# Performance work log

Hardware: AMD Instinct MI355X
Metric: run time of the kernel (lower is better)

## Reference

```python
import jax, jax.numpy as jnp
import numpy as np
import math

B, S, DM, H, N_HASHES, BUCKET = 1, 1024, 512, 8, 8, 64
HD = DM // H
N_BUCKETS = max(2, 2 * (S // (2 * BUCKET)))   # 16
ROT = max(1, N_BUCKETS // 2)                  # 8


def setup_inputs() -> dict:
    key = jax.random.key(0)
    ks = jax.random.split(key, 6)
    sc = 1.0 / math.sqrt(DM)
    return {
        "x": jax.random.normal(ks[0], (B, S, DM), dtype=jnp.float32),
        "w_qk": (jax.random.normal(ks[1], (DM, DM), dtype=jnp.float32) * sc),
        "b_qk": jnp.zeros((DM,), dtype=jnp.float32),
        "w_v": (jax.random.normal(ks[2], (DM, DM), dtype=jnp.float32) * sc),
        "b_v": jnp.zeros((DM,), dtype=jnp.float32),
        "w_o": (jax.random.normal(ks[3], (DM, DM), dtype=jnp.float32) * sc),
        "b_o": jnp.zeros((DM,), dtype=jnp.float32),
        # random rotations used for LSH hashing (torch.randn in hash_vectors)
        "rotations": jax.random.normal(ks[4], (N_HASHES, H, HD, ROT), dtype=jnp.float32),
    }


def reference(x, w_qk, b_qk, w_v, b_v, w_o, b_o, rotations):
    # projections, split heads: (B, H, S, HD)
    qk = (x @ w_qk + b_qk).reshape(B, S, H, HD).transpose(0, 2, 1, 3)
    v = (x @ w_v + b_v).reshape(B, S, H, HD).transpose(0, 2, 1, 3)

    # LSH bucket assignment: (B, H, S, n_hashes)
    rot = jnp.einsum('bhnd,rhdc->bhnrc', qk, rotations)
    rot = jnp.concatenate([rot, -rot], axis=-1)
    buckets = jnp.argmax(rot, axis=-1)

    # The original gathers (batch, head, pos) jointly per bucket, so attention
    # mixes across batch and head; flatten exactly the same way.
    N = B * H * S
    qkf = qk.reshape(N, HD)
    vf = v.reshape(N, HD)
    bkf = buckets.reshape(N, N_HASHES).T  # (n_hashes, N)

    # dots are shared across hash rounds; only the bucket mask changes
    dots = (qkf @ qkf.T) / math.sqrt(HD)  # (N, N)

    def body(acc, bk):
        same = bk[:, None] == bk[None, :]  # bucket-equality mask
        w = jax.nn.softmax(jnp.where(same, dots, -jnp.inf), axis=-1)
        return acc + w @ vf, None

    out, _ = jax.lax.scan(body, jnp.zeros_like(vf), bkf)
    out = out / N_HASHES

    out = out.reshape(B, H, S, HD).transpose(0, 2, 1, 3).reshape(B, S, DM)
    return out @ w_o + b_o
```

## Files before the change

kernel.cpp:

```cpp
#include <hip/hip_runtime.h>
#include <math.h>

#define S 1024
#define DM 512
#define H 8
#define HD 64
#define NH 8
#define NB 16
#define N 8192
#define SCALE 0.125f
#define EXP2C 0.18033688f

typedef __attribute__((ext_vector_type(4))) float f32x4;
typedef __attribute__((ext_vector_type(8))) short s16x8;
typedef __attribute__((ext_vector_type(4))) short s16x4;

__device__ __forceinline__ short f2bf(float f) {
  union { float f; unsigned u; } a; a.f = f;
  unsigned r = a.u + 0x7fffu + ((a.u >> 16) & 1u);
  return (short)(r >> 16);
}
__device__ __forceinline__ float bf2f(short h) {
  union { unsigned u; float f; } a; a.u = ((unsigned)(unsigned short)h) << 16;
  return a.f;
}
__device__ __forceinline__ int f2bf2(float lo, float hi) {
  return (int)(unsigned short)f2bf(lo) | (((int)f2bf(hi)) << 16);
}

#if __has_builtin(__builtin_amdgcn_mfma_f32_16x16x16_bf16)
#define MFMA_PV(a, b, c) __builtin_amdgcn_mfma_f32_16x16x16_bf16(a, b, c, 0, 0, 0)
#else
#define MFMA_PV(a, b, c) __builtin_amdgcn_mfma_f32_16x16x16bf16_1k(a, b, c, 0, 0, 0)
#endif

__global__ __launch_bounds__(256) void wprep_kernel(
    const float* __restrict__ wqk, const float* __restrict__ wv,
    const float* __restrict__ wo, const float* __restrict__ x,
    short* __restrict__ wtqk, short* __restrict__ wtv, short* __restrict__ wto,
    short* __restrict__ xs, int* __restrict__ cz) {
  int tid = threadIdx.x;
  if (blockIdx.x == 0) cz[tid] = 0;
  if (blockIdx.x >= 192) {
    int xb = blockIdx.x - 192;
    size_t base = ((size_t)xb * 256 + tid) * 16;
    const float4* xp = (const float4*)(x + base);
    float4 f0 = xp[0], f1 = xp[1], f2 = xp[2], f3 = xp[3];
    float vv[16] = {f0.x,f0.y,f0.z,f0.w, f1.x,f1.y,f1.z,f1.w,
                    f2.x,f2.y,f2.z,f2.w, f3.x,f3.y,f3.z,f3.w};
    s16x8 h0[2], h1[2], h2[2];
#pragma unroll
    for (int g = 0; g < 2; ++g)
#pragma unroll
      for (int i = 0; i < 8; ++i) {
        float v = vv[g * 8 + i];
        short a = f2bf(v); float r1 = v - bf2f(a);
        short b = f2bf(r1); short c = f2bf(r1 - bf2f(b));
        h0[g][i] = a; h1[g][i] = b; h2[g][i] = c;
      }
    s16x8* p0 = (s16x8*)(xs + base);
    s16x8* p1 = (s16x8*)(xs + (size_t)S * DM + base);
    s16x8* p2 = (s16x8*)(xs + (size_t)2 * S * DM + base);
    p0[0] = h0[0]; p0[1] = h0[1];
    p1[0] = h1[0]; p1[1] = h1[1];
    p2[0] = h2[0]; p2[1] = h2[1];
    return;
  }
  int mat = blockIdx.x >> 6;
  int tile = blockIdx.x & 63;
  int kt = tile >> 3, dt = tile & 7;
  const float* w = (mat == 0) ? wqk : ((mat == 1) ? wv : wo);

  __shared__ float wlds[64 * 68];
  int kr = tid >> 2, c4 = tid & 3;
  const float4* src = (const float4*)(w + (size_t)(kt * 64 + kr) * DM + dt * 64 + c4 * 16);
#pragma unroll
  for (int i = 0; i < 4; ++i) {
    float4 v = src[i];
    float* d = &wlds[kr * 68 + c4 * 16 + i * 4];
    d[0] = v.x; d[1] = v.y; d[2] = v.z; d[3] = v.w;
  }
  __syncthreads();
  int dr = tid >> 2, kc = tid & 3;
  s16x8 h0a, h0b, h1a, h1b, h2a, h2b;
#pragma unroll
  for (int i = 0; i < 8; ++i) {
    float v = wlds[(kc * 16 + i) * 68 + dr];
    short a = f2bf(v); float r1 = v - bf2f(a);
    short b = f2bf(r1); short c = f2bf(r1 - bf2f(b));
    h0a[i] = a; h1a[i] = b; h2a[i] = c;
  }
#pragma unroll
  for (int i = 0; i < 8; ++i) {
    float v = wlds[(kc * 16 + 8 + i) * 68 + dr];
    short a = f2bf(v); float r1 = v - bf2f(a);
    short b = f2bf(r1); short c = f2bf(r1 - bf2f(b));
    h0b[i] = a; h1b[i] = b; h2b[i] = c;
  }
  size_t dst = (size_t)(dt * 64 + dr) * DM + kt * 64 + kc * 16;
  if (mat == 0) {
    s16x8* p0 = (s16x8*)(wtqk + dst);
    s16x8* p1 = (s16x8*)(wtqk + (size_t)DM * DM + dst);
    s16x8* p2 = (s16x8*)(wtqk + (size_t)2 * DM * DM + dst);
    p0[0] = h0a; p0[1] = h0b; p1[0] = h1a; p1[1] = h1b; p2[0] = h2a; p2[1] = h2b;
  } else if (mat == 1) {
    s16x8* p = (s16x8*)(wtv + dst); p[0] = h0a; p[1] = h0b;
  } else {
    s16x8* p = (s16x8*)(wto + dst); p[0] = h0a; p[1] = h0b;
  }
}

#define PST 72
__global__ __launch_bounds__(256) void projmm_kernel(
    const short* __restrict__ xs, const short* __restrict__ wtqk,
    const short* __restrict__ wtv,
    const float* __restrict__ bqk, const float* __restrict__ bv,
    float* __restrict__ qkpart, short* __restrict__ vb) {
  int mt = blockIdx.x & 15;
  int rest = blockIdx.x >> 4;
  int sp = rest >> 3;
  int head = rest & 7;
  bool isv = (sp == 6);
  int xl = isv ? 0 : ((0x210100 >> (sp << 2)) & 0xF);
  int wl = isv ? 0 : ((0x012010 >> (sp << 2)) & 0xF);
  const short* wt = isv ? wtv : (wtqk + (size_t)wl * DM * DM);
  const short* xsl = xs + (size_t)xl * S * DM;

  __shared__ short a_lds[2][64 * PST];
  __shared__ short b_lds[2][64 * PST];

  int tid = threadIdx.x;
  int wave = tid >> 6, lane = tid & 63;
  int col = lane & 15, quad = lane >> 4;
  int mh = wave & 1, nh2 = wave >> 1;

  f32x4 acc[2][2];
#pragma unroll
  for (int i = 0; i < 2; ++i)
#pragma unroll
    for (int j = 0; j < 2; ++j) acc[i][j] = (f32x4){0.f, 0.f, 0.f, 0.f};

  int sr = tid >> 2, c4 = tid & 3;
  int gran = sr * PST + ((c4 ^ (sr & 3)) << 4);

  {
    const s16x8* xp = (const s16x8*)(xsl + (size_t)(mt * 64 + sr) * DM + c4 * 16);
    s16x8* ad = (s16x8*)&a_lds[0][gran];
    ad[0] = xp[0]; ad[1] = xp[1];
    const s16x8* wp = (const s16x8*)(wt + (size_t)(head * 64 + sr) * DM + c4 * 16);
    s16x8* bd = (s16x8*)&b_lds[0][gran];
    bd[0] = wp[0]; bd[1] = wp[1];
  }
  __syncthreads();

  for (int ci = 0; ci < 8; ++ci) {
    int cur = ci & 1, nxt = cur ^ 1;
    s16x8 px0, px1, pw0, pw1;
    bool has = (ci + 1) < 8;
    if (has) {
      int kc = ci + 1;
      const s16x8* xp = (const s16x8*)(xsl + (size_t)(mt * 64 + sr) * DM + kc * 64 + c4 * 16);
      px0 = xp[0]; px1 = xp[1];
      const s16x8* wp = (const s16x8*)(wt + (size_t)(head * 64 + sr) * DM + kc * 64 + c4 * 16);
      pw0 = wp[0]; pw1 = wp[1];
    }
#pragma unroll
    for (int s2 = 0; s2 < 2; ++s2) {
      s16x8 af[2], bfv[2];
#pragma unroll
      for (int mi = 0; mi < 2; ++mi) {
        int row = mh * 32 + mi * 16 + col;
        int cidx = ((s2 << 1) + (quad >> 1)) ^ (row & 3);
        af[mi] = *(const s16x8*)&a_lds[cur][row * PST + (cidx << 4) + ((quad & 1) << 3)];
      }
#pragma unroll
      for (int ni = 0; ni < 2; ++ni) {
        int row = nh2 * 32 + ni * 16 + col;
        int cidx = ((s2 << 1) + (quad >> 1)) ^ (row & 3);
        bfv[ni] = *(const s16x8*)&b_lds[cur][row * PST + (cidx << 4) + ((quad & 1) << 3)];
      }
#pragma unroll
      for (int mi = 0; mi < 2; ++mi)
#pragma unroll
        for (int ni = 0; ni < 2; ++ni)
          acc[mi][ni] = __builtin_amdgcn_mfma_f32_16x16x32_bf16(af[mi], bfv[ni],
                                                               acc[mi][ni], 0, 0, 0);
    }
    if (has) {
      s16x8* ad = (s16x8*)&a_lds[nxt][gran];
      ad[0] = px0; ad[1] = px1;
      s16x8* bd = (s16x8*)&b_lds[nxt][gran];
      bd[0] = pw0; bd[1] = pw1;
    }
    __syncthreads();
  }
  if (isv) {
#pragma unroll
    for (int ni = 0; ni < 2; ++ni) {
      int nl = nh2 * 32 + ni * 16 + col;
      float bb = bv[head * 64 + nl];
#pragma unroll
      for (int mi = 0; mi < 2; ++mi)
#pragma unroll
        for (int u = 0; u < 4; ++u) {
          int s = mt * 64 + mh * 32 + mi * 16 + quad * 4 + u;
          vb[((size_t)head * S + s) * HD + nl] = f2bf(acc[mi][ni][u] + bb);
        }
    }
  } else {
    float* dst = qkpart + (size_t)sp * N * HD;
#pragma unroll
    for (int ni = 0; ni < 2; ++ni) {
      int nl = nh2 * 32 + ni * 16 + col;
      float bb = (sp == 0) ? bqk[head * 64 + nl] : 0.f;
#pragma unroll
      for (int mi = 0; mi < 2; ++mi)
#pragma unroll
        for (int u = 0; u < 4; ++u) {
          int s = mt * 64 + mh * 32 + mi * 16 + quad * 4 + u;
          dst[((size_t)head * S + s) * HD + nl] = acc[mi][ni][u] + bb;
        }
    }
  }
}

__global__ __launch_bounds__(256) void sumslab_kernel(
    const float* __restrict__ qkpart, float* __restrict__ qkf,
    short* __restrict__ qkb) {
  int idx = blockIdx.x * 256 + threadIdx.x;
  f32x4 s = ((const f32x4*)qkpart)[idx];
#pragma unroll
  for (int sl = 1; sl < 6; ++sl)
    s += ((const f32x4*)(qkpart + (size_t)sl * N * HD))[idx];
  ((f32x4*)qkf)[idx] = s;
  int2 pk = make_int2(f2bf2(s[0], s[1]), f2bf2(s[2], s[3]));
  *(int2*)(qkb + (size_t)idx * 4) = pk;
}

__global__ __launch_bounds__(256) void bucket_kernel(
    const float* __restrict__ qkf, const float* __restrict__ rot,
    int* __restrict__ cursor, int* __restrict__ perm2) {
  __shared__ float Rl[HD * 8];
  __shared__ int lcnt[NB];
  __shared__ int gbase[NB];
  int tid = threadIdx.x;
  int g = blockIdx.x * 256 + tid;
  int n = g & (N - 1);
  int r = g >> 13;
  int h = n >> 10;
  const float* R = rot + (size_t)((r * H + h) * HD) * 8;
  if (tid < 128) ((f32x4*)Rl)[tid] = ((const f32x4*)R)[tid];
  if (tid < NB) lcnt[tid] = 0;

  f32x4 qv[16];
  const f32x4* q4 = (const f32x4*)(qkf + (size_t)n * HD);
#pragma unroll
  for (int d4 = 0; d4 < 16; ++d4) qv[d4] = q4[d4];
  __syncthreads();

  float v[8];
#pragma unroll
  for (int c = 0; c < 8; ++c) v[c] = 0.f;
#pragma unroll
  for (int d4 = 0; d4 < 16; ++d4) {
    f32x4 q = qv[d4];
#pragma unroll
    for (int j = 0; j < 4; ++j) {
      const f32x4* Rr = (const f32x4*)&Rl[(d4 * 4 + j) * 8];
      f32x4 r0 = Rr[0], r1 = Rr[1];
      float qj = q[j];
#pragma unroll
      for (int c = 0; c < 4; ++c) v[c] = fmaf(qj, r0[c], v[c]);
#pragma unroll
      for (int c = 0; c < 4; ++c) v[4 + c] = fmaf(qj, r1[c], v[4 + c]);
    }
  }
  float best = v[0];
  int bi = 0;
#pragma unroll
  for (int c = 1; c < 16; ++c) {
    float val = (c < 8) ? v[c] : -v[c - 8];
    if (val > best) { best = val; bi = c; }
  }

  int lrank = atomicAdd(&lcnt[bi], 1);
  __syncthreads();
  if (tid < NB) gbase[tid] = atomicAdd(&cursor[(r << 4) + tid], lcnt[tid]);
  __syncthreads();
  perm2[(((size_t)(r << 4) + bi) << 13) + gbase[bi] + lrank] = n;
}

#define KT 64
#define KST 72
#define VTS2 72
#define VBUF (64 * VTS2)
__global__ __launch_bounds__(512) void attn_kernel(
    const short* __restrict__ qkb, const short* __restrict__ vb,
    const int* __restrict__ perm2, const int* __restrict__ cursor,
    short* __restrict__ accumB) {
  int bx = blockIdx.x;
  int rb = bx & 127;
  int chunk = bx >> 7;
  int r = rb >> 4;
  int cnt = cursor[rb];
  int q0 = chunk << 7;
  if (q0 >= cnt) return;
  const int* plist = perm2 + ((size_t)rb << 13);

  int tid = threadIdx.x;
  int wave = tid >> 6, lane = tid & 63;
  int col = lane & 15, quad = lane >> 4;

  __shared__ short k_lds[2][KT * KST];
  __shared__ short v_lds[2][VBUF];

  int qslot = q0 + (wave << 4) + col;
  bool qvalid = qslot < cnt;
  int qidx = plist[qvalid ? qslot : 0];
  bool wactive = (q0 + (wave << 4)) < cnt;

  for (int e = tid; e < VBUF; e += 512) ((int*)v_lds)[e] = 0;

  s16x8 qa[2];
#pragma unroll
  for (int s2 = 0; s2 < 2; ++s2)
    qa[s2] = *(const s16x8*)(qkb + (size_t)qidx * HD + s2 * 32 + quad * 8);
  __syncthreads();

  float lsum = 0.f;
  f32x4 o0 = {0,0,0,0}, o1 = {0,0,0,0}, o2 = {0,0,0,0}, o3 = {0,0,0,0};

  int jsk = tid >> 2, csk = tid & 3;
  bool stager = tid < 256;
  int kgran = jsk * KST + ((csk ^ (jsk & 3)) << 4);
  int ksw0 = (jsk + 16 * csk) & 63;
  int ksw1 = (jsk + 16 * csk + 4) & 63;
  int vdr = csk * 16 * VTS2;

  int vrow = col * VTS2;
  int vco = (col >> 3) << 2;

  {
    int nj = min(KT, cnt);
    if (stager && jsk < nj) {
      int gk = plist[jsk];
      const s16x8* kp = (const s16x8*)(qkb + (size_t)gk * HD + (csk << 4));
      const s16x8* vp = (const s16x8*)(vb + (size_t)gk * HD + (csk << 4));
      s16x8 a0 = kp[0], a1 = kp[1], b0 = vp[0], b1 = vp[1];
      s16x8* kd = (s16x8*)&k_lds[0][kgran];
      kd[0] = a0; kd[1] = a1;
      short* vt = &v_lds[0][vdr];
#pragma unroll
      for (int i = 0; i < 8; ++i) {
        vt[i * VTS2 + ksw0] = b0[i];
        vt[(8 + i) * VTS2 + ksw1] = b1[i];
      }
    }
  }
  int pln = 0; bool pln_ok = false;
  if (stager) {
    int i1 = KT + jsk;
    pln_ok = i1 < cnt;
    pln = plist[i1 < 8192 ? i1 : 8191];
  }
  __syncthreads();

  int ntiles = (cnt + KT - 1) >> 6;
  for (int t = 0; t < ntiles; ++t) {
    int jt = t << 6;
    int cur = t & 1, nxt = cur ^ 1;
    s16x8 a0, a1, b0, b1;
    bool pf_ok = stager && pln_ok;
    if (pf_ok) {
      const s16x8* kp = (const s16x8*)(qkb + (size_t)pln * HD + (csk << 4));
      const s16x8* vp = (const s16x8*)(vb + (size_t)pln * HD + (csk << 4));
      a0 = kp[0]; a1 = kp[1]; b0 = vp[0]; b1 = vp[1];
    }
    int pl2 = 0; bool pl2_ok = false;
    if (stager) {
      int i2 = jt + 2 * KT + jsk;
      pl2_ok = i2 < cnt;
      pl2 = plist[i2 < 8192 ? i2 : 8191];
    }
    if (wactive) {
      const short* vtc = v_lds[cur];
      const short* ktc = k_lds[cur];
      f32x4 sA = {0,0,0,0}, sB = {0,0,0,0}, sC = {0,0,0,0}, sD = {0,0,0,0};
#define QK1(C, SA) { int key = ((C) << 4) + col; \
      const short* kb = &ktc[key * KST]; \
      { int cidx = (quad >> 1) ^ (key & 3); \
        s16x8 kf = *(const s16x8*)&kb[(cidx << 4) + ((quad & 1) << 3)]; \
        SA = __builtin_amdgcn_mfma_f32_16x16x32_bf16(kf, qa[0], SA, 0, 0, 0); } \
      { int cidx = (2 + (quad >> 1)) ^ (key & 3); \
        s16x8 kf = *(const s16x8*)&kb[(cidx << 4) + ((quad & 1) << 3)]; \
        SA = __builtin_amdgcn_mfma_f32_16x16x32_bf16(kf, qa[1], SA, 0, 0, 0); } }
      __builtin_amdgcn_s_setprio(1);
      QK1(0, sA) QK1(1, sB) QK1(2, sC) QK1(3, sD)
      __builtin_amdgcn_s_setprio(0);
      s16x4 p0, p1, p2, p3;
#define SM1(C, SA, PF) { int kbase = jt + ((C) << 4) + (quad << 2); \
      float pw[4]; \
      if (kbase + 4 <= cnt) { \
        _Pragma("unroll") for (int u = 0; u < 4; ++u) pw[u] = exp2f(SA[u] * EXP2C); \
      } else { \
        _Pragma("unroll") for (int u = 0; u < 4; ++u) \
          pw[u] = (kbase + u < cnt) ? exp2f(SA[u] * EXP2C) : 0.f; \
      } \
      lsum += (pw[0] + pw[1]) + (pw[2] + pw[3]); \
      int dA_, dB_; \
      asm("v_cvt_pk_bf16_f32 %0, %1, %2" : "=v"(dA_) : "v"(pw[0]), "v"(pw[1])); \
      asm("v_cvt_pk_bf16_f32 %0, %1, %2" : "=v"(dB_) : "v"(pw[2]), "v"(pw[3])); \
      ((int*)&PF)[0] = dA_; ((int*)&PF)[1] = dB_; }
      SM1(0, sA, p0) SM1(1, sB, p1) SM1(2, sC, p2) SM1(3, sD, p3)
#define PV1(C, PF) { int k0s = ((C) << 4) + (quad << 2) + vco; \
      s16x4 va = *(const s16x4*)&vtc[vrow + (k0s & 63)]; \
      s16x4 vb_ = *(const s16x4*)&vtc[16 * VTS2 + vrow + ((k0s + 16) & 63)]; \
      s16x4 vc = *(const s16x4*)&vtc[32 * VTS2 + vrow + ((k0s + 32) & 63)]; \
      s16x4 vd = *(const s16x4*)&vtc[48 * VTS2 + vrow + ((k0s + 48) & 63)]; \
      o0 = MFMA_PV(PF, va, o0); o1 = MFMA_PV(PF, vb_, o1); \
      o2 = MFMA_PV(PF, vc, o2); o3 = MFMA_PV(PF, vd, o3); }
      __builtin_amdgcn_s_setprio(1);
      PV1(0, p0) PV1(1, p1) PV1(2, p2) PV1(3, p3)
      __builtin_amdgcn_s_setprio(0);
#undef QK1
#undef SM1
#undef PV1
    }
    if (pf_ok) {
      s16x8* kd = (s16x8*)&k_lds[nxt][kgran];
      kd[0] = a0; kd[1] = a1;
      short* vt = &v_lds[nxt][vdr];
#pragma unroll
      for (int i = 0; i < 8; ++i) {
        vt[i * VTS2 + ksw0] = b0[i];
        vt[(8 + i) * VTS2 + ksw1] = b1[i];
      }
    }
    pln = pl2; pln_ok = pl2_ok;
    __syncthreads();
  }

  lsum += __shfl_xor(lsum, 16);
  lsum += __shfl_xor(lsum, 32);
  float inv = 1.f / lsum;
#pragma unroll
  for (int u = 0; u < 4; ++u) {
    int slot = (quad << 2) + u;
    int spos = q0 + (wave << 4) + slot;
    float inv_u = __shfl(inv, slot);
    int qidx_u = __shfl(qidx, slot);
    if (spos < cnt) {
      short* dst = accumB + ((size_t)r * N + qidx_u) * HD + col;
      dst[0]  = f2bf(o0[u] * inv_u);
      dst[16] = f2bf(o1[u] * inv_u);
      dst[32] = f2bf(o2[u] * inv_u);
      dst[48] = f2bf(o3[u] * inv_u);
    }
  }
}

__global__ __launch_bounds__(256) void asum_kernel(
    const short* __restrict__ accumB, short* __restrict__ asumB) {
  size_t idx = (size_t)blockIdx.x * 256 + threadIdx.x;
  float a[8];
#pragma unroll
  for (int i = 0; i < 8; ++i) a[i] = 0.f;
#pragma unroll
  for (int r = 0; r < NH; ++r) {
    s16x8 h = *(const s16x8*)(accumB + (size_t)r * N * HD + idx * 8);
#pragma unroll
    for (int i = 0; i < 8; ++i) a[i] += bf2f(h[i]);
  }
  s16x8 o;
#pragma unroll
  for (int i = 0; i < 8; ++i) o[i] = f2bf(a[i] * 0.125f);
  *(s16x8*)(asumB + idx * 8) = o;
}

__global__ __launch_bounds__(256) void outproj_kernel(
    const short* __restrict__ asumB, const short* __restrict__ wto,
    const float* __restrict__ bo, float* __restrict__ out) {
  int mt = blockIdx.x & 31;
  int nt = blockIdx.x >> 5;
  __shared__ short a_lds[2][32 * PST];
  __shared__ short b_lds[2][64 * PST];
  int tid = threadIdx.x;
  int wave = tid >> 6, lane = tid & 63;
  int col = lane & 15, quad = lane >> 4;
  int mi2 = wave & 1, nh2 = wave >> 1;

  f32x4 acc[2];
  acc[0] = (f32x4){0.f,0.f,0.f,0.f};
  acc[1] = (f32x4){0.f,0.f,0.f,0.f};

  bool isA = tid < 128;
  int sr = tid >> 2, c4 = tid & 3;
  int agran = sr * PST + ((c4 ^ (sr & 3)) << 4);
  int dl = (tid - 128) >> 1, gp = tid & 1;

  {
    if (isA) {
      const s16x8* ap = (const s16x8*)(asumB + ((size_t)0 * S + mt * 32 + sr) * HD + c4 * 16);
      s16x8* ad = (s16x8*)&a_lds[0][agran];
      ad[0] = ap[0]; ad[1] = ap[1];
    } else {
      const s16x8* wp = (const s16x8*)(wto + (size_t)(nt * 64 + dl) * DM + gp * 32);
      int g0 = gp * 2;
      s16x8* d0 = (s16x8*)&b_lds[0][dl * PST + ((g0 ^ (dl & 3)) << 4)];
      d0[0] = wp[0]; d0[1] = wp[1];
      s16x8* d1 = (s16x8*)&b_lds[0][dl * PST + (((g0 + 1) ^ (dl & 3)) << 4)];
      d1[0] = wp[2]; d1[1] = wp[3];
    }
  }
  __syncthreads();

  for (int kc = 0; kc < 8; ++kc) {
    int cur = kc & 1, nxt = cur ^ 1;
    bool has = kc + 1 < 8;
    s16x8 pa0, pa1, pb0, pb1, pb2, pb3;
    if (has) {
      if (isA) {
        const s16x8* ap = (const s16x8*)(asumB +
            ((size_t)(kc + 1) * S + mt * 32 + sr) * HD + c4 * 16);
        pa0 = ap[0]; pa1 = ap[1];
      } else {
        const s16x8* wp = (const s16x8*)(wto + (size_t)(nt * 64 + dl) * DM +
                                         (kc + 1) * 64 + gp * 32);
        pb0 = wp[0]; pb1 = wp[1]; pb2 = wp[2]; pb3 = wp[3];
      }
    }
#pragma unroll
    for (int s2 = 0; s2 < 2; ++s2) {
      int arow = mi2 * 16 + col;
      int acidx = ((s2 << 1) + (quad >> 1)) ^ (arow & 3);
      s16x8 af = *(const s16x8*)&a_lds[cur][arow * PST + (acidx << 4) + ((quad & 1) << 3)];
      s16x8 bfv[2];
#pragma unroll
      for (int ni = 0; ni < 2; ++ni) {
        int brow = nh2 * 32 + ni * 16 + col;
        int bcidx = ((s2 << 1) + (quad >> 1)) ^ (brow & 3);
        bfv[ni] = *(const s16x8*)&b_lds[cur][brow * PST + (bcidx << 4) + ((quad & 1) << 3)];
      }
#pragma unroll
      for (int ni = 0; ni < 2; ++ni)
        acc[ni] = __builtin_amdgcn_mfma_f32_16x16x32_bf16(af, bfv[ni], acc[ni], 0, 0, 0);
    }
    if (has) {
      if (isA) {
        s16x8* ad = (s16x8*)&a_lds[nxt][agran];
        ad[0] = pa0; ad[1] = pa1;
      } else {
        int g0 = gp * 2;
        s16x8* d0 = (s16x8*)&b_lds[nxt][dl * PST + ((g0 ^ (dl & 3)) << 4)];
        d0[0] = pb0; d0[1] = pb1;
        s16x8* d1 = (s16x8*)&b_lds[nxt][dl * PST + (((g0 + 1) ^ (dl & 3)) << 4)];
        d1[0] = pb2; d1[1] = pb3;
      }
    }
    __syncthreads();
  }
#pragma unroll
  for (int ni = 0; ni < 2; ++ni) {
    int nl = nh2 * 32 + ni * 16 + col;
    int dgl = nt * 64 + nl;
    float bb = bo[dgl];
#pragma unroll
    for (int u = 0; u < 4; ++u) {
      int s = mt * 32 + mi2 * 16 + quad * 4 + u;
      out[(size_t)s * DM + dgl] = acc[ni][u] + bb;
    }
  }
}

extern "C" void kernel_launch(void* const* d_in, const int* in_sizes, int n_in,
                              void* d_out, int out_size, void* d_ws, size_t ws_size,
                              hipStream_t stream) {
  const float* x    = (const float*)d_in[0];
  const float* w_qk = (const float*)d_in[1];
  const float* b_qk = (const float*)d_in[2];
  const float* w_v  = (const float*)d_in[3];
  const float* b_v  = (const float*)d_in[4];
  const float* w_o  = (const float*)d_in[5];
  const float* b_o  = (const float*)d_in[6];
  const float* rot  = (const float*)d_in[7];
  float* out = (float*)d_out;

  char* ws = (char*)d_ws;
  const size_t MB = 1024u * 1024u;
  short* qkb    = (short*)(ws);
  short* vb     = (short*)(ws + 1 * MB);
  float* qkpart = (float*)(ws + 2 * MB);
  short* accumB = (short*)(ws + 2 * MB);
  int* perm2    = (int*)(ws + 10 * MB);
  float* qkf    = (float*)(ws + 18 * MB);
  short* wtqk   = (short*)(ws + 20 * MB);
  short* wtv    = (short*)(ws + 20 * MB + 1536u * 1024);
  short* wto    = (short*)(ws + 22 * MB);
  int* cursor   = (int*)(ws + 22 * MB + 512u * 1024);
  short* xs     = (short*)(ws + 23 * MB);
  short* asumB  = (short*)(ws + 26 * MB);

  wprep_kernel<<<320, 256, 0, stream>>>(w_qk, w_v, w_o, x, wtqk, wtv, wto, xs, cursor);
  projmm_kernel<<<896, 256, 0, stream>>>(xs, wtqk, wtv, b_qk, b_v, qkpart, vb);
  sumslab_kernel<<<512, 256, 0, stream>>>(qkpart, qkf, qkb);
  bucket_kernel<<<(NH * N) / 256, 256, 0, stream>>>(qkf, rot, cursor, perm2);
  attn_kernel<<<64 * 128, 512, 0, stream>>>(qkb, vb, perm2, cursor, accumB);
  asum_kernel<<<256, 256, 0, stream>>>(accumB, asumB);
  outproj_kernel<<<256, 256, 0, stream>>>(asumB, wto, b_o, out);
}
```

Before: 135.2 us.

## Process two query tiles per wave in attention to reuse K/V LDS fragments

Halves the attention block to 256 threads (4 waves), with each wave now handling 32 queries as two 16-row tiles that share every K and V fragment read from LDS. All threads take part in staging, so the separate stager-thread predicate goes away. The aim is to cut LDS reads per MFMA and give each wave more independent MFMA work. In exchange, register pressure roughly doubles for accumulators and P fragments, and with fewer waves per block there is less latency hiding per block.

```diff
diff --git a/kernel.cpp b/kernel.cpp
--- a/kernel.cpp
+++ b/kernel.cpp
@@ -294,7 +294,7 @@
 #define KST 72
 #define VTS2 72
 #define VBUF (64 * VTS2)
-__global__ __launch_bounds__(512) void attn_kernel(
+__global__ __launch_bounds__(256) void attn_kernel(
     const short* __restrict__ qkb, const short* __restrict__ vb,
     const int* __restrict__ perm2, const int* __restrict__ cursor,
     short* __restrict__ accumB) {
@@ -314,24 +314,27 @@
   __shared__ short k_lds[2][KT * KST];
   __shared__ short v_lds[2][VBUF];
 
-  int qslot = q0 + (wave << 4) + col;
-  bool qvalid = qslot < cnt;
-  int qidx = plist[qvalid ? qslot : 0];
-  bool wactive = (q0 + (wave << 4)) < cnt;
-
-  for (int e = tid; e < VBUF; e += 512) ((int*)v_lds)[e] = 0;
-
-  s16x8 qa[2];
-#pragma unroll
-  for (int s2 = 0; s2 < 2; ++s2)
-    qa[s2] = *(const s16x8*)(qkb + (size_t)qidx * HD + s2 * 32 + quad * 8);
-  __syncthreads();
-
-  float lsum = 0.f;
-  f32x4 o0 = {0,0,0,0}, o1 = {0,0,0,0}, o2 = {0,0,0,0}, o3 = {0,0,0,0};
+  int qlo = q0 + (wave << 5) + col;
+  int qhi = qlo + 16;
+  int qidxL = plist[qlo < cnt ? qlo : 0];
+  int qidxH = plist[qhi < cnt ? qhi : 0];
+  bool wactive = (q0 + (wave << 5)) < cnt;
+
+  for (int e = tid; e < VBUF; e += 256) ((int*)v_lds)[e] = 0;
+
+  s16x8 qaL[2], qaH[2];
+#pragma unroll
+  for (int s2 = 0; s2 < 2; ++s2) {
+    qaL[s2] = *(const s16x8*)(qkb + (size_t)qidxL * HD + s2 * 32 + quad * 8);
+    qaH[s2] = *(const s16x8*)(qkb + (size_t)qidxH * HD + s2 * 32 + quad * 8);
+  }
+  __syncthreads();
+
+  float lsumL = 0.f, lsumH = 0.f;
+  f32x4 oL0 = {0,0,0,0}, oL1 = {0,0,0,0}, oL2 = {0,0,0,0}, oL3 = {0,0,0,0};
+  f32x4 oH0 = {0,0,0,0}, oH1 = {0,0,0,0}, oH2 = {0,0,0,0}, oH3 = {0,0,0,0};
 
   int jsk = tid >> 2, csk = tid & 3;
-  bool stager = tid < 256;
   int kgran = jsk * KST + ((csk ^ (jsk & 3)) << 4);
   int ksw0 = (jsk + 16 * csk) & 63;
   int ksw1 = (jsk + 16 * csk + 4) & 63;
@@ -342,7 +345,7 @@
 
   {
     int nj = min(KT, cnt);
-    if (stager && jsk < nj) {
+    if (jsk < nj) {
       int gk = plist[jsk];
       const s16x8* kp = (const s16x8*)(qkb + (size_t)gk * HD + (csk << 4));
       const s16x8* vp = (const s16x8*)(vb + (size_t)gk * HD + (csk << 4));
@@ -358,7 +361,7 @@
     }
   }
   int pln = 0; bool pln_ok = false;
-  if (stager) {
+  {
     int i1 = KT + jsk;
     pln_ok = i1 < cnt;
     pln = plist[i1 < 8192 ? i1 : 8191];
@@ -370,14 +373,14 @@
     int jt = t << 6;
     int cur = t & 1, nxt = cur ^ 1;
     s16x8 a0, a1, b0, b1;
-    bool pf_ok = stager && pln_ok;
+    bool pf_ok = pln_ok;
     if (pf_ok) {
       const s16x8* kp = (const s16x8*)(qkb + (size_t)pln * HD + (csk << 4));
       const s16x8* vp = (const s16x8*)(vb + (size_t)pln * HD + (csk << 4));
       a0 = kp[0]; a1 = kp[1]; b0 = vp[0]; b1 = vp[1];
     }
     int pl2 = 0; bool pl2_ok = false;
-    if (stager) {
+    {
       int i2 = jt + 2 * KT + jsk;
       pl2_ok = i2 < cnt;
       pl2 = plist[i2 < 8192 ? i2 : 8191];
@@ -386,19 +389,22 @@
       const short* vtc = v_lds[cur];
       const short* ktc = k_lds[cur];
       f32x4 sA = {0,0,0,0}, sB = {0,0,0,0}, sC = {0,0,0,0}, sD = {0,0,0,0};
-#define QK1(C, SA) { int key = ((C) << 4) + col; \
+      f32x4 hA = {0,0,0,0}, hB = {0,0,0,0}, hC = {0,0,0,0}, hD = {0,0,0,0};
+#define QK1(C, SL, SH) { int key = ((C) << 4) + col; \
       const short* kb = &ktc[key * KST]; \
       { int cidx = (quad >> 1) ^ (key & 3); \
         s16x8 kf = *(const s16x8*)&kb[(cidx << 4) + ((quad & 1) << 3)]; \
-        SA = __builtin_amdgcn_mfma_f32_16x16x32_bf16(kf, qa[0], SA, 0, 0, 0); } \
+        SL = __builtin_amdgcn_mfma_f32_16x16x32_bf16(kf, qaL[0], SL, 0, 0, 0); \
+        SH = __builtin_amdgcn_mfma_f32_16x16x32_bf16(kf, qaH[0], SH, 0, 0, 0); } \
       { int cidx = (2 + (quad >> 1)) ^ (key & 3); \
         s16x8 kf = *(const s16x8*)&kb[(cidx << 4) + ((quad & 1) << 3)]; \
-        SA = __builtin_amdgcn_mfma_f32_16x16x32_bf16(kf, qa[1], SA, 0, 0, 0); } }
+        SL = __builtin_amdgcn_mfma_f32_16x16x32_bf16(kf, qaL[1], SL, 0, 0, 0); \
+        SH = __builtin_amdgcn_mfma_f32_16x16x32_bf16(kf, qaH[1], SH, 0, 0, 0); } }
       __builtin_amdgcn_s_setprio(1);
-      QK1(0, sA) QK1(1, sB) QK1(2, sC) QK1(3, sD)
+      QK1(0, sA, hA) QK1(1, sB, hB) QK1(2, sC, hC) QK1(3, sD, hD)
       __builtin_amdgcn_s_setprio(0);
-      s16x4 p0, p1, p2, p3;
-#define SM1(C, SA, PF) { int kbase = jt + ((C) << 4) + (quad << 2); \
+      s16x4 pL0, pL1, pL2, pL3, pH0, pH1, pH2, pH3;
+#define SM1(C, SA, PF, LS) { int kbase = jt + ((C) << 4) + (quad << 2); \
       float pw[4]; \
       if (kbase + 4 <= cnt) { \
         _Pragma("unroll") for (int u = 0; u < 4; ++u) pw[u] = exp2f(SA[u] * EXP2C); \
@@ -406,21 +412,26 @@
         _Pragma("unroll") for (int u = 0; u < 4; ++u) \
           pw[u] = (kbase + u < cnt) ? exp2f(SA[u] * EXP2C) : 0.f; \
       } \
-      lsum += (pw[0] + pw[1]) + (pw[2] + pw[3]); \
+      LS += (pw[0] + pw[1]) + (pw[2] + pw[3]); \
       int dA_, dB_; \
       asm("v_cvt_pk_bf16_f32 %0, %1, %2" : "=v"(dA_) : "v"(pw[0]), "v"(pw[1])); \
       asm("v_cvt_pk_bf16_f32 %0, %1, %2" : "=v"(dB_) : "v"(pw[2]), "v"(pw[3])); \
       ((int*)&PF)[0] = dA_; ((int*)&PF)[1] = dB_; }
-      SM1(0, sA, p0) SM1(1, sB, p1) SM1(2, sC, p2) SM1(3, sD, p3)
-#define PV1(C, PF) { int k0s = ((C) << 4) + (quad << 2) + vco; \
+      SM1(0, sA, pL0, lsumL) SM1(1, sB, pL1, lsumL)
+      SM1(2, sC, pL2, lsumL) SM1(3, sD, pL3, lsumL)
+      SM1(0, hA, pH0, lsumH) SM1(1, hB, pH1, lsumH)
+      SM1(2, hC, pH2, lsumH) SM1(3, hD, pH3, lsumH)
+#define PV1(C, PFL, PFH) { int k0s = ((C) << 4) + (quad << 2) + vco; \
       s16x4 va = *(const s16x4*)&vtc[vrow + (k0s & 63)]; \
       s16x4 vb_ = *(const s16x4*)&vtc[16 * VTS2 + vrow + ((k0s + 16) & 63)]; \
       s16x4 vc = *(const s16x4*)&vtc[32 * VTS2 + vrow + ((k0s + 32) & 63)]; \
       s16x4 vd = *(const s16x4*)&vtc[48 * VTS2 + vrow + ((k0s + 48) & 63)]; \
-      o0 = MFMA_PV(PF, va, o0); o1 = MFMA_PV(PF, vb_, o1); \
-      o2 = MFMA_PV(PF, vc, o2); o3 = MFMA_PV(PF, vd, o3); }
+      oL0 = MFMA_PV(PFL, va, oL0); oH0 = MFMA_PV(PFH, va, oH0); \
+      oL1 = MFMA_PV(PFL, vb_, oL1); oH1 = MFMA_PV(PFH, vb_, oH1); \
+      oL2 = MFMA_PV(PFL, vc, oL2); oH2 = MFMA_PV(PFH, vc, oH2); \
+      oL3 = MFMA_PV(PFL, vd, oL3); oH3 = MFMA_PV(PFH, vd, oH3); }
       __builtin_amdgcn_s_setprio(1);
-      PV1(0, p0) PV1(1, p1) PV1(2, p2) PV1(3, p3)
+      PV1(0, pL0, pH0) PV1(1, pL1, pH1) PV1(2, pL2, pH2) PV1(3, pL3, pH3)
       __builtin_amdgcn_s_setprio(0);
 #undef QK1
 #undef SM1
@@ -440,21 +451,38 @@
     __syncthreads();
   }
 
-  lsum += __shfl_xor(lsum, 16);
-  lsum += __shfl_xor(lsum, 32);
-  float inv = 1.f / lsum;
+  lsumL += __shfl_xor(lsumL, 16);
+  lsumL += __shfl_xor(lsumL, 32);
+  lsumH += __shfl_xor(lsumH, 16);
+  lsumH += __shfl_xor(lsumH, 32);
+  float invL = 1.f / lsumL;
+  float invH = 1.f / lsumH;
 #pragma unroll
   for (int u = 0; u < 4; ++u) {
     int slot = (quad << 2) + u;
-    int spos = q0 + (wave << 4) + slot;
-    float inv_u = __shfl(inv, slot);
-    int qidx_u = __shfl(qidx, slot);
-    if (spos < cnt) {
-      short* dst = accumB + ((size_t)r * N + qidx_u) * HD + col;
-      dst[0]  = f2bf(o0[u] * inv_u);
-      dst[16] = f2bf(o1[u] * inv_u);
-      dst[32] = f2bf(o2[u] * inv_u);
-      dst[48] = f2bf(o3[u] * inv_u);
+    int sposL = q0 + (wave << 5) + slot;
+    float invL_u = __shfl(invL, slot);
+    int qidxL_u = __shfl(qidxL, slot);
+    if (sposL < cnt) {
+      short* dst = accumB + ((size_t)r * N + qidxL_u) * HD + col;
+      dst[0]  = f2bf(oL0[u] * invL_u);
+      dst[16] = f2bf(oL1[u] * invL_u);
+      dst[32] = f2bf(oL2[u] * invL_u);
+      dst[48] = f2bf(oL3[u] * invL_u);
+    }
+  }
+#pragma unroll
+  for (int u = 0; u < 4; ++u) {
+    int slot = (quad << 2) + u;
+    int sposH = q0 + (wave << 5) + 16 + slot;
+    float invH_u = __shfl(invH, slot);
+    int qidxH_u = __shfl(qidxH, slot);
+    if (sposH < cnt) {
+      short* dst = accumB + ((size_t)r * N + qidxH_u) * HD + col;
+      dst[0]  = f2bf(oH0[u] * invH_u);
+      dst[16] = f2bf(oH1[u] * invH_u);
+      dst[32] = f2bf(oH2[u] * invH_u);
+      dst[48] = f2bf(oH3[u] * invH_u);
     }
   }
 }
@@ -604,7 +632,7 @@
   projmm_kernel<<<896, 256, 0, stream>>>(xs, wtqk, wtv, b_qk, b_v, qkpart, vb);
   sumslab_kernel<<<512, 256, 0, stream>>>(qkpart, qkf, qkb);
   bucket_kernel<<<(NH * N) / 256, 256, 0, stream>>>(qkf, rot, cursor, perm2);
-  attn_kernel<<<64 * 128, 512, 0, stream>>>(qkb, vb, perm2, cursor, accumB);
+  attn_kernel<<<64 * 128, 256, 0, stream>>>(qkb, vb, perm2, cursor, accumB);
   asum_kernel<<<256, 256, 0, stream>>>(accumB, asumB);
   outproj_kernel<<<256, 256, 0, stream>>>(asumB, wto, b_o, out);
 }
```

After: 150.0 us. +10.9%, slower.

## Split attention key range across two blocks and merge partial sums in asum

Applied to the files above, without the earlier changes.

Each attention work item is split into two blocks, each covering half of the key tiles of the bucket. The blocks write unnormalized bf16 partial outputs and fp32 partial denominators to separate slabs. The asum kernel then adds both halves and normalizes before averaging over hash rounds. This aims to raise the number of active blocks and shorten the serial key loop, at the cost of extra intermediate memory traffic and bf16 rounding of unnormalized partials.

```diff
diff --git a/kernel.cpp b/kernel.cpp
--- a/kernel.cpp
+++ b/kernel.cpp
@@ -297,15 +297,23 @@
 __global__ __launch_bounds__(512) void attn_kernel(
     const short* __restrict__ qkb, const short* __restrict__ vb,
     const int* __restrict__ perm2, const int* __restrict__ cursor,
-    short* __restrict__ accumB) {
+    short* __restrict__ accumB, float* __restrict__ denF) {
   int bx = blockIdx.x;
   int rb = bx & 127;
-  int chunk = bx >> 7;
+  int khalf = (bx >> 7) & 1;
+  int chunk = bx >> 8;
   int r = rb >> 4;
   int cnt = cursor[rb];
   int q0 = chunk << 7;
   if (q0 >= cnt) return;
   const int* plist = perm2 + ((size_t)rb << 13);
+
+  int ntiles = (cnt + KT - 1) >> 6;
+  int htiles = (ntiles + 1) >> 1;
+  int t0 = khalf ? htiles : 0;
+  int t1 = khalf ? ntiles : htiles;
+  int kend = min(cnt, t1 << 6);
+  int j0 = t0 << 6;
 
   int tid = threadIdx.x;
   int wave = tid >> 6, lane = tid & 63;
@@ -341,9 +349,9 @@
   int vco = (col >> 3) << 2;
 
   {
-    int nj = min(KT, cnt);
+    int nj = min(KT, kend - j0);
     if (stager && jsk < nj) {
-      int gk = plist[jsk];
+      int gk = plist[j0 + jsk];
       const s16x8* kp = (const s16x8*)(qkb + (size_t)gk * HD + (csk << 4));
       const s16x8* vp = (const s16x8*)(vb + (size_t)gk * HD + (csk << 4));
       s16x8 a0 = kp[0], a1 = kp[1], b0 = vp[0], b1 = vp[1];
@@ -359,16 +367,16 @@
   }
   int pln = 0; bool pln_ok = false;
   if (stager) {
-    int i1 = KT + jsk;
-    pln_ok = i1 < cnt;
+    int i1 = j0 + KT + jsk;
+    pln_ok = i1 < kend;
     pln = plist[i1 < 8192 ? i1 : 8191];
   }
   __syncthreads();
 
-  int ntiles = (cnt + KT - 1) >> 6;
-  for (int t = 0; t < ntiles; ++t) {
+  for (int t = t0; t < t1; ++t) {
     int jt = t << 6;
-    int cur = t & 1, nxt = cur ^ 1;
+    int ti = t - t0;
+    int cur = ti & 1, nxt = cur ^ 1;
     s16x8 a0, a1, b0, b1;
     bool pf_ok = stager && pln_ok;
     if (pf_ok) {
@@ -379,7 +387,7 @@
     int pl2 = 0; bool pl2_ok = false;
     if (stager) {
       int i2 = jt + 2 * KT + jsk;
-      pl2_ok = i2 < cnt;
+      pl2_ok = i2 < kend;
       pl2 = plist[i2 < 8192 ? i2 : 8191];
     }
     if (wactive) {
@@ -442,34 +450,40 @@
 
   lsum += __shfl_xor(lsum, 16);
   lsum += __shfl_xor(lsum, 32);
-  float inv = 1.f / lsum;
+  if (quad == 0 && qvalid)
+    denF[((size_t)khalf * NH + r) * N + qidx] = lsum;
+  short* slab = accumB + (size_t)khalf * NH * N * HD;
 #pragma unroll
   for (int u = 0; u < 4; ++u) {
     int slot = (quad << 2) + u;
     int spos = q0 + (wave << 4) + slot;
-    float inv_u = __shfl(inv, slot);
     int qidx_u = __shfl(qidx, slot);
     if (spos < cnt) {
-      short* dst = accumB + ((size_t)r * N + qidx_u) * HD + col;
-      dst[0]  = f2bf(o0[u] * inv_u);
-      dst[16] = f2bf(o1[u] * inv_u);
-      dst[32] = f2bf(o2[u] * inv_u);
-      dst[48] = f2bf(o3[u] * inv_u);
+      short* dst = slab + ((size_t)r * N + qidx_u) * HD + col;
+      dst[0]  = f2bf(o0[u]);
+      dst[16] = f2bf(o1[u]);
+      dst[32] = f2bf(o2[u]);
+      dst[48] = f2bf(o3[u]);
     }
   }
 }
 
 __global__ __launch_bounds__(256) void asum_kernel(
-    const short* __restrict__ accumB, short* __restrict__ asumB) {
+    const short* __restrict__ accumB, const float* __restrict__ denF,
+    short* __restrict__ asumB) {
   size_t idx = (size_t)blockIdx.x * 256 + threadIdx.x;
+  int n = (int)(idx >> 3);
   float a[8];
 #pragma unroll
   for (int i = 0; i < 8; ++i) a[i] = 0.f;
 #pragma unroll
   for (int r = 0; r < NH; ++r) {
-    s16x8 h = *(const s16x8*)(accumB + (size_t)r * N * HD + idx * 8);
-#pragma unroll
-    for (int i = 0; i < 8; ++i) a[i] += bf2f(h[i]);
+    s16x8 h0 = *(const s16x8*)(accumB + (size_t)r * N * HD + idx * 8);
+    s16x8 h1 = *(const s16x8*)(accumB + ((size_t)NH + r) * N * HD + idx * 8);
+    float d = denF[(size_t)r * N + n] + denF[((size_t)NH + r) * N + n];
+    float inv = 1.f / d;
+#pragma unroll
+    for (int i = 0; i < 8; ++i) a[i] += (bf2f(h0[i]) + bf2f(h1[i])) * inv;
   }
   s16x8 o;
 #pragma unroll
@@ -590,7 +604,6 @@
   short* qkb    = (short*)(ws);
   short* vb     = (short*)(ws + 1 * MB);
   float* qkpart = (float*)(ws + 2 * MB);
-  short* accumB = (short*)(ws + 2 * MB);
   int* perm2    = (int*)(ws + 10 * MB);
   float* qkf    = (float*)(ws + 18 * MB);
   short* wtqk   = (short*)(ws + 20 * MB);
@@ -599,12 +612,15 @@
   int* cursor   = (int*)(ws + 22 * MB + 512u * 1024);
   short* xs     = (short*)(ws + 23 * MB);
   short* asumB  = (short*)(ws + 26 * MB);
+  short* accumB = (short*)(ws + 32 * MB);
+  float* denF   = (float*)(ws + 48 * MB);
 
   wprep_kernel<<<320, 256, 0, stream>>>(w_qk, w_v, w_o, x, wtqk, wtv, wto, xs, cursor);
   projmm_kernel<<<896, 256, 0, stream>>>(xs, wtqk, wtv, b_qk, b_v, qkpart, vb);
   sumslab_kernel<<<512, 256, 0, stream>>>(qkpart, qkf, qkb);
   bucket_kernel<<<(NH * N) / 256, 256, 0, stream>>>(qkf, rot, cursor, perm2);
-  attn_kernel<<<64 * 128, 512, 0, stream>>>(qkb, vb, perm2, cursor, accumB);
-  asum_kernel<<<256, 256, 0, stream>>>(accumB, asumB);
+  attn_kernel<<<64 * 2 * 128, 512, 0, stream>>>(qkb, vb, perm2, cursor,
+                                                accumB, denF);
+  asum_kernel<<<256, 256, 0, stream>>>(accumB, denF, asumB);
   outproj_kernel<<<256, 256, 0, stream>>>(asumB, wto, b_o, out);
 }
```

After: 136.0 us. About the same (+0.6%).
